# Optimization experiments

Hardware: AMD Instinct MI355X
Metric: run time of the kernel (lower is better)

Reference implementation:

```python
import jax, jax.numpy as jnp
import numpy as np

DIM = 128
HEADS = 4
GN_GROUPS = 4
EPS = 1e-5


def setup_inputs() -> dict:
    key = jax.random.key(0)
    ks = jax.random.split(key, 6)
    B, C, H, W = 4, DIM, 64, 64
    x = jax.random.normal(ks[0], (B, C, H, W), dtype=jnp.float32)
    # 1x1 convs are channel matmuls: store as [out_ch, in_ch]
    w_qkv = jax.random.normal(ks[1], (3 * C, C), dtype=jnp.float32) * (C ** -0.5)
    w_out = jax.random.normal(ks[2], (C, C), dtype=jnp.float32) * (C ** -0.5)
    b_out = jax.random.normal(ks[3], (C,), dtype=jnp.float32) * 0.01
    gn_gamma = jnp.ones((C,), dtype=jnp.float32)
    gn_beta = jnp.zeros((C,), dtype=jnp.float32)
    return {"x": x, "w_qkv": w_qkv, "w_out": w_out, "b_out": b_out,
            "gn_gamma": gn_gamma, "gn_beta": gn_beta}


def _attention_block(x, w_qkv, w_out, b_out, gn_gamma, gn_beta):
    b, c, h, w = x.shape
    d = c // HEADS
    scale = d ** -0.5
    # 1x1 conv == per-pixel matmul over channels
    qkv = jnp.einsum('bchw,oc->bohw', x, w_qkv)  # [b, 3c, h, w]
    q, k, v = jnp.split(qkv, 3, axis=1)
    # 'b (h d) x y -> b h (x y) d'
    def to_heads(t):
        return t.reshape(b, HEADS, d, h * w).transpose(0, 1, 3, 2)  # [b, H, N, d]
    q, k, v = to_heads(q), to_heads(k), to_heads(v)
    dots = jnp.einsum('bhnd,bhmd->bhnm', q, k) * scale  # [b, H, N, N]
    attn = jax.nn.softmax(dots, axis=-1)
    out = jnp.einsum('bhnm,bhmd->bhnd', attn, v)  # [b, H, N, d]
    # 'b h (x y) d -> b (h d) x y'
    out = out.transpose(0, 1, 3, 2).reshape(b, c, h, w)
    # output 1x1 conv + bias
    out = jnp.einsum('bchw,oc->bohw', out, w_out) + b_out[None, :, None, None]
    # GroupNorm(4, c)
    g = out.reshape(b, GN_GROUPS, c // GN_GROUPS, h, w)
    mean = g.mean(axis=(2, 3, 4), keepdims=True)
    var = g.var(axis=(2, 3, 4), keepdims=True)
    g = (g - mean) * jax.lax.rsqrt(var + EPS)
    out = g.reshape(b, c, h, w) * gn_gamma[None, :, None, None] + gn_beta[None, :, None, None]
    return out + x


def reference(x, w_qkv, w_out, b_out, gn_gamma, gn_beta):
    return _attention_block(x, w_qkv, w_out, b_out, gn_gamma, gn_beta)
```

## Files before the change

### kernel.cpp

```cpp
#include <hip/hip_runtime.h>

#define DIM   128
#define NPIX  4096
#define DHEAD 32

using u16 = unsigned short;
typedef __attribute__((ext_vector_type(8))) short   short8;
typedef __attribute__((ext_vector_type(8))) u16     ushort8;
typedef __attribute__((ext_vector_type(4))) float   floatx4;
typedef __attribute__((ext_vector_type(2))) unsigned int uint2v;

#define SCL 0.25513899f

__device__ __forceinline__ float bf2f(u16 u) {
  union { unsigned int i; float f; } v; v.i = ((unsigned int)u) << 16; return v.f;
}
__device__ __forceinline__ u16 f2bf(float f) {
  union { unsigned int i; float f; } v; v.f = f;
  unsigned int i = v.i;
  return (u16)((i + 0x7FFFu + ((i >> 16) & 1u)) >> 16);
}
__device__ __forceinline__ unsigned int pk2bf(float a, float b) {
  union { float f; unsigned int u; } ua, ub; ua.f = a; ub.f = b;
  return __builtin_amdgcn_perm(ub.u, ua.u, 0x07060302u);
}

template<bool F32> __device__ __forceinline__ float ld1(const void* p, size_t i) {
  if constexpr (F32) return ((const float*)p)[i];
  else               return bf2f(((const u16*)p)[i]);
}
template<bool F32> __device__ __forceinline__ float4 ld4(const void* p, size_t i) {
  if constexpr (F32) {
    return *(const float4*)((const float*)p + i);
  } else {
    const ushort4 u = *(const ushort4*)((const u16*)p + i);
    return make_float4(bf2f(u.x), bf2f(u.y), bf2f(u.z), bf2f(u.w));
  }
}
template<bool F32> __device__ __forceinline__ void st4(void* p, size_t i, float4 v) {
  if constexpr (F32) {
    *(float4*)((float*)p + i) = v;
  } else {
    ushort4 u; u.x = f2bf(v.x); u.y = f2bf(v.y); u.z = f2bf(v.z); u.w = f2bf(v.w);
    *(ushort4*)((u16*)p + i) = u;
  }
}

__global__ void k_detect(const u16* __restrict__ x, int* __restrict__ flag,
                         float* __restrict__ S) {
  if (threadIdx.x < 40) S[threadIdx.x] = 0.f;
  if (threadIdx.x == 0 && blockIdx.x == 0) {
    int big = 0;
    for (int i = 0; i < 128; ++i) {
      const float v = bf2f(x[i]);
      if (!(fabsf(v) < 1e4f)) big = 1;
    }
    *flag = big;
  }
}

template<bool F32>
__global__ __launch_bounds__(256) void k_qkv(const void* __restrict__ x,
                                             const void* __restrict__ wqkv,
                                             u16* __restrict__ Q,
                                             u16* __restrict__ K,
                                             u16* __restrict__ V,
                                             const int* __restrict__ flag) {
  if (*flag != (F32 ? 1 : 0)) return;
  const int b = blockIdx.z, y = blockIdx.y, pt = blockIdx.x;
  const int tl = threadIdx.x;
  __shared__ float Ws[32 * 129];
  if (y < 8) {
    const int m = y >> 2, h = y & 3;
    const int ddq = tl & 3, pw = tl >> 2;
    const int rb = m * DIM + h * 32;
    for (int i = tl; i < 32 * DIM; i += 256)
      Ws[(i >> 7) * 129 + (i & 127)] =
          ld1<F32>(wqkv, (size_t)(rb + (i >> 7)) * DIM + (i & 127));
    __syncthreads();
    const int p0 = pt * 256 + pw * 4;
    float acc[8][4];
#pragma unroll
    for (int j = 0; j < 8; ++j) { acc[j][0] = acc[j][1] = acc[j][2] = acc[j][3] = 0.f; }
    const size_t xb = (size_t)b * DIM * NPIX + p0;
    for (int c = 0; c < DIM; ++c) {
      const float4 xv = ld4<F32>(x, xb + (size_t)c * NPIX);
#pragma unroll
      for (int j = 0; j < 8; ++j) {
        const float wv = Ws[(ddq * 8 + j) * 129 + c];
        acc[j][0] += wv * xv.x; acc[j][1] += wv * xv.y;
        acc[j][2] += wv * xv.z; acc[j][3] += wv * xv.w;
      }
    }
    u16* dst = (m == 0) ? Q : K;
    const float scl = (m == 0) ? 1.f : SCL;
    const int bh = b * 4 + h;
#pragma unroll
    for (int t = 0; t < 4; ++t) {
      ushort8 w8;
#pragma unroll
      for (int j = 0; j < 8; ++j) w8[j] = f2bf(acc[j][t] * scl);
      *(ushort8*)(dst + ((size_t)bh * NPIX + p0 + t) * DHEAD + ddq * 8) = w8;
    }
  } else {
    const int og = (y - 8) * 4 + (pt >> 2);
    const int ptv = pt & 3;
    for (int i = tl; i < 8 * DIM; i += 256)
      Ws[(i >> 7) * 129 + (i & 127)] =
          ld1<F32>(wqkv, (size_t)(2 * DIM + og * 8 + (i >> 7)) * DIM + (i & 127));
    __syncthreads();
    const int p0 = ptv * 1024 + tl * 4;
    float acc[8][4];
#pragma unroll
    for (int j = 0; j < 8; ++j) { acc[j][0] = acc[j][1] = acc[j][2] = acc[j][3] = 0.f; }
    const size_t xb = (size_t)b * DIM * NPIX + p0;
    for (int c = 0; c < DIM; ++c) {
      const float4 xv = ld4<F32>(x, xb + (size_t)c * NPIX);
#pragma unroll
      for (int j = 0; j < 8; ++j) {
        const float wv = Ws[j * 129 + c];
        acc[j][0] += wv * xv.x; acc[j][1] += wv * xv.y;
        acc[j][2] += wv * xv.z; acc[j][3] += wv * xv.w;
      }
    }
#pragma unroll
    for (int j = 0; j < 8; ++j) {
      const int c = og * 8 + j;
      ushort4 w4;
      w4.x = f2bf(acc[j][0]); w4.y = f2bf(acc[j][1]);
      w4.z = f2bf(acc[j][2]); w4.w = f2bf(acc[j][3]);
      *(ushort4*)(V + ((size_t)b * DIM + c) * NPIX + p0) = w4;
    }
  }
}

__device__ __forceinline__ short8 xform_p(unsigned c0, unsigned c1,
                                          unsigned c2, unsigned c3) {
  uint2v sw = __builtin_amdgcn_permlane32_swap(c0, c2, false, false);
  uint2v sx = __builtin_amdgcn_permlane16_swap(sw[0], sw[1], false, false);
  uint2v sy = __builtin_amdgcn_permlane32_swap(c1, c3, false, false);
  uint2v sz = __builtin_amdgcn_permlane16_swap(sy[0], sy[1], false, false);
  union { unsigned u[4]; short8 s; } r;
  r.u[0] = sx[0]; r.u[1] = sz[0]; r.u[2] = sx[1]; r.u[3] = sz[1];
  return r.s;
}

__global__ __launch_bounds__(512) void k_attn(const u16* __restrict__ Q,
                                              const u16* __restrict__ K,
                                              const u16* __restrict__ V,
                                              u16* __restrict__ O) {
  const int id = blockIdx.y * 32 + blockIdx.x;
  const int nid = (id & 7) * 64 + (id >> 3);
  const int bh = nid >> 5, qb = nid & 31;
  const int tid = threadIdx.x;
  const int wv = tid >> 6, lane = tid & 63;
  const int quad = lane >> 4, l15 = lane & 15;
  const int b = bh >> 2, h = bh & 3;

  __shared__ __align__(16) u16 Vlds[2][32 * 136];
  __shared__ __align__(16) u16 Olds[32 * 136];

  const int qtok0 = qb * 128 + wv * 16 + l15;
  const short8 qf = *(const short8*)(Q + ((size_t)bh * NPIX + qtok0) * DHEAD + quad * 8);

  floatx4 o00 = {0.f, 0.f, 0.f, 0.f}, o01 = {0.f, 0.f, 0.f, 0.f};
  floatx4 ol  = {0.f, 0.f, 0.f, 0.f};
  const short8 onesf = {(short)0x3F80, (short)0x3F80, (short)0x3F80, (short)0x3F80,
                        (short)0x3F80, (short)0x3F80, (short)0x3F80, (short)0x3F80};

  const u16* Ka = K + ((size_t)bh * NPIX + l15) * DHEAD + quad * 8;

  const int sdd = tid >> 4, soc = tid & 15;
  const u16* Vg = V + ((size_t)(b * DIM + h * DHEAD + sdd)) * NPIX + soc * 8;
  u16* Vd0 = Vlds[0] + sdd * 136 + soc * 8;
  u16* Vd1 = Vlds[1] + sdd * 136 + soc * 8;

  *(ushort8*)Vd0 = *(const ushort8*)Vg;

  for (int ch = 0; ch < 32; ++ch) {
    const int cur = ch & 1;
    ushort8 kf[8];
#pragma unroll
    for (int sub = 0; sub < 8; ++sub)
      kf[sub] = *(const ushort8*)(Ka + (size_t)(ch * 128 + sub * 16) * DHEAD);
    __syncthreads();
    ushort8 vpre;
    if (ch + 1 < 32) vpre = *(const ushort8*)(Vg + (ch + 1) * 128);
#pragma unroll
    for (int kc = 0; kc < 4; ++kc) {
      unsigned ca[4];
#pragma unroll
      for (int s = 0; s < 2; ++s) {
        const int sub = kc * 2 + s;
        union { ushort8 u; short8 s8; } afc; afc.u = kf[sub];
        const floatx4 s0 = __builtin_amdgcn_mfma_f32_16x16x32_bf16(
            afc.s8, qf, (floatx4){0.f, 0.f, 0.f, 0.f}, 0, 0, 0);
        const float a0 = __builtin_amdgcn_exp2f(s0[0]);
        const float a1 = __builtin_amdgcn_exp2f(s0[1]);
        const float a2 = __builtin_amdgcn_exp2f(s0[2]);
        const float a3 = __builtin_amdgcn_exp2f(s0[3]);
        ca[s * 2 + 0] = pk2bf(a0, a1); ca[s * 2 + 1] = pk2bf(a2, a3);
      }
      const short8 pa = xform_p(ca[0], ca[1], ca[2], ca[3]);
      const short8 vb0 = *(const short8*)(Vlds[cur] + l15 * 136 + kc * 32 + quad * 8);
      const short8 vb1 = *(const short8*)(Vlds[cur] + (16 + l15) * 136 + kc * 32 + quad * 8);
      __builtin_amdgcn_s_setprio(1);
      o00 = __builtin_amdgcn_mfma_f32_16x16x32_bf16(pa, vb0, o00, 0, 0, 0);
      o01 = __builtin_amdgcn_mfma_f32_16x16x32_bf16(pa, vb1, o01, 0, 0, 0);
      ol  = __builtin_amdgcn_mfma_f32_16x16x32_bf16(pa, onesf, ol, 0, 0, 0);
      __builtin_amdgcn_s_setprio(0);
    }
    if (ch + 1 < 32) {
      *(ushort8*)(cur ? Vd0 : Vd1) = vpre;
    }
  }
  float li[4];
#pragma unroll
  for (int r = 0; r < 4; ++r) li[r] = 1.f / ol[r];
  uint2v w00, w01;
  w00[0] = (unsigned)f2bf(o00[0] * li[0]) | ((unsigned)f2bf(o00[1] * li[1]) << 16);
  w00[1] = (unsigned)f2bf(o00[2] * li[2]) | ((unsigned)f2bf(o00[3] * li[3]) << 16);
  w01[0] = (unsigned)f2bf(o01[0] * li[0]) | ((unsigned)f2bf(o01[1] * li[1]) << 16);
  w01[1] = (unsigned)f2bf(o01[2] * li[2]) | ((unsigned)f2bf(o01[3] * li[3]) << 16);
  __syncthreads();
  *(uint2v*)(Olds + l15 * 136 + wv * 16 + quad * 4) = w00;
  *(uint2v*)(Olds + (16 + l15) * 136 + wv * 16 + quad * 4) = w01;
  __syncthreads();
  const int d = tid >> 4, oc = tid & 15;
  u16* og = O + ((size_t)(b * DIM + h * DHEAD + d)) * NPIX + qb * 128;
  *(ushort8*)(og + oc * 8) = *(const ushort8*)(Olds + d * 136 + oc * 8);
}

template<bool F32>
__global__ __launch_bounds__(256) void k_proj(const u16* __restrict__ O,
                                              const void* __restrict__ wout,
                                              const void* __restrict__ bout,
                                              float* __restrict__ Y,
                                              float* __restrict__ Sred,
                                              const int* __restrict__ flag) {
  if (*flag != (F32 ? 1 : 0)) return;
  const int b = blockIdx.z, og = blockIdx.y, pt = blockIdx.x;
  const int tl = threadIdx.x;
  __shared__ float Ws[8][DIM];
  __shared__ __align__(16) u16 Olds[2][16][520];
  for (int i = tl; i < 8 * DIM; i += 256)
    Ws[i >> 7][i & 127] = ld1<F32>(wout, (size_t)(og * 8 + (i >> 7)) * DIM + (i & 127));
  const u16* Ob = O + (size_t)b * DIM * NPIX + pt * 512;
  const int srow = tl >> 6;
  const int scol = (tl & 63) * 8;
#pragma unroll
  for (int s = 0; s < 4; ++s) {
    const int r = s * 4 + srow;
    *(ushort8*)(&Olds[0][r][scol]) = *(const ushort8*)(Ob + (size_t)r * NPIX + scol);
  }
  float acc[8][2];
#pragma unroll
  for (int j = 0; j < 8; ++j) { acc[j][0] = acc[j][1] = 0.f; }
  for (int chv = 0; chv < 8; ++chv) {
    const int cur = chv & 1;
    __syncthreads();
    ushort8 pre[4];
    if (chv + 1 < 8) {
      const u16* gb = Ob + (size_t)(chv + 1) * 16 * NPIX;
#pragma unroll
      for (int s = 0; s < 4; ++s)
        pre[s] = *(const ushort8*)(gb + (size_t)(s * 4 + srow) * NPIX + scol);
    }
#pragma unroll
    for (int cc = 0; cc < 16; ++cc) {
      const int c = chv * 16 + cc;
      const ushort2 xv2 = *(const ushort2*)(&Olds[cur][cc][tl * 2]);
      const float x0 = bf2f(xv2.x), x1 = bf2f(xv2.y);
#pragma unroll
      for (int j = 0; j < 8; ++j) {
        const float wv = Ws[j][c];
        acc[j][0] += wv * x0; acc[j][1] += wv * x1;
      }
    }
    if (chv + 1 < 8) {
      const int nxt = cur ^ 1;
#pragma unroll
      for (int s = 0; s < 4; ++s)
        *(ushort8*)(&Olds[nxt][s * 4 + srow][scol]) = pre[s];
    }
  }
  const int p0 = pt * 512 + tl * 2;
  float s1 = 0.f, s2 = 0.f;
#pragma unroll
  for (int j = 0; j < 8; ++j) {
    const int o = og * 8 + j;
    const float bo = ld1<F32>(bout, o);
    float2 y2;
    y2.x = acc[j][0] + bo; y2.y = acc[j][1] + bo;
    *(float2*)(Y + ((size_t)b * DIM + o) * NPIX + p0) = y2;
    s1 += y2.x + y2.y;
    s2 += y2.x * y2.x + y2.y * y2.y;
  }
  __shared__ float red[2][256];
  red[0][tl] = s1; red[1][tl] = s2;
  __syncthreads();
  for (int off = 128; off >= 1; off >>= 1) {
    if (tl < off) { red[0][tl] += red[0][tl + off]; red[1][tl] += red[1][tl + off]; }
    __syncthreads();
  }
  if (tl == 0) {
    const int g = og >> 2;
    atomicAdd(&Sred[(b * 4 + g) * 2 + 0], red[0][0]);
    atomicAdd(&Sred[(b * 4 + g) * 2 + 1], red[1][0]);
  }
}

template<bool F32>
__global__ __launch_bounds__(256) void k_gn(const float* __restrict__ Y,
                                            const float* __restrict__ Sred,
                                            const void* __restrict__ x,
                                            const void* __restrict__ gamma,
                                            const void* __restrict__ beta,
                                            void* __restrict__ out,
                                            const int* __restrict__ flag) {
  if (*flag != (F32 ? 1 : 0)) return;
  const int idx = (blockIdx.x * 256 + threadIdx.x) * 4;
  const int b = idx >> 19;
  const int c = (idx >> 12) & 127;
  const int g = c >> 5;
  const float inv_n = 1.f / (32.f * 4096.f);
  const float s1 = Sred[(b * 4 + g) * 2 + 0];
  const float s2 = Sred[(b * 4 + g) * 2 + 1];
  const float mean = s1 * inv_n;
  const float var = s2 * inv_n - mean * mean;
  const float rs = rsqrtf(var + 1e-5f);
  const float ga = ld1<F32>(gamma, c) * rs;
  const float be = ld1<F32>(beta, c) - mean * ga;
  const float4 y4 = *(const float4*)(Y + idx);
  const float4 xv = ld4<F32>(x, idx);
  float4 r;
  r.x = y4.x * ga + be + xv.x;
  r.y = y4.y * ga + be + xv.y;
  r.z = y4.z * ga + be + xv.z;
  r.w = y4.w * ga + be + xv.w;
  st4<F32>(out, idx, r);
}

extern "C" void kernel_launch(void* const* d_in, const int* in_sizes, int n_in,
                              void* d_out, int out_size, void* d_ws, size_t ws_size,
                              hipStream_t stream) {
  const void* x     = d_in[0];
  const void* wqkv  = d_in[1];
  const void* wout  = d_in[2];
  const void* bout  = d_in[3];
  const void* gamma = d_in[4];
  const void* beta  = d_in[5];
  char* ws = (char*)d_ws;
  u16*   Q = (u16*)(ws + ((size_t)0  << 20));
  u16*   K = (u16*)(ws + ((size_t)8  << 20));
  u16*   V = (u16*)(ws + ((size_t)16 << 20));
  u16*   O = (u16*)(ws + ((size_t)24 << 20));
  float* Y = (float*)(ws + ((size_t)32 << 20));
  float* S = (float*)(ws + ((size_t)40 << 20));
  int*   F = (int*)(ws + ((size_t)40 << 20) + 128);

  k_detect<<<1, 64, 0, stream>>>((const u16*)x, F, S);

  k_qkv<false><<<dim3(16, 12, 4), 256, 0, stream>>>(x, wqkv, Q, K, V, F);
  k_qkv<true> <<<dim3(16, 12, 4), 256, 0, stream>>>(x, wqkv, Q, K, V, F);
  k_attn<<<dim3(32, 16), 512, 0, stream>>>(Q, K, V, O);
  k_proj<false><<<dim3(8, 16, 4), 256, 0, stream>>>(O, wout, bout, Y, S, F);
  k_proj<true> <<<dim3(8, 16, 4), 256, 0, stream>>>(O, wout, bout, Y, S, F);
  k_gn<false><<<2048, 256, 0, stream>>>(Y, S, x, gamma, beta, d_out, F);
  k_gn<true> <<<2048, 256, 0, stream>>>(Y, S, x, gamma, beta, d_out, F);
}
```

Measured before the change: 192.6 us.

## Split attention keys across waves and reduce partial outputs through LDS

The attention kernel previously gave each wave 16 query rows and streamed all keys, with V staged through double-buffered LDS and a barrier every chunk. Now each wave holds all 128 queries of the block in registers and handles its own slice of the keys, reading K and V straight from global memory without LDS staging or per-chunk barriers. The partial outputs and row sums of the eight waves are then added up serially in LDS, with a barrier per wave, before normalisation and the bf16 store. This removes the inner-loop barriers, but it greatly raises register pressure (24 accumulators plus 8 Q fragments), lowers occupancy, and adds a serialized eight-step reduction at the end.

```diff
diff --git a/kernel.cpp b/kernel.cpp
--- a/kernel.cpp
+++ b/kernel.cpp
@@ -157,78 +157,94 @@
   const int quad = lane >> 4, l15 = lane & 15;
   const int b = bh >> 2, h = bh & 3;
 
-  __shared__ __align__(16) u16 Vlds[2][32 * 136];
-  __shared__ __align__(16) u16 Olds[32 * 136];
-
-  const int qtok0 = qb * 128 + wv * 16 + l15;
-  const short8 qf = *(const short8*)(Q + ((size_t)bh * NPIX + qtok0) * DHEAD + quad * 8);
-
-  floatx4 o00 = {0.f, 0.f, 0.f, 0.f}, o01 = {0.f, 0.f, 0.f, 0.f};
-  floatx4 ol  = {0.f, 0.f, 0.f, 0.f};
+  __shared__ __align__(16) float Ob[32][132];
+  __shared__ __align__(16) float Lb[128];
+
+  short8 qf[8];
+#pragma unroll
+  for (int f = 0; f < 8; ++f)
+    qf[f] = *(const short8*)(Q + ((size_t)bh * NPIX + qb * 128 + f * 16 + l15) * DHEAD + quad * 8);
+
+  floatx4 o[8][2], ol[8];
+#pragma unroll
+  for (int f = 0; f < 8; ++f) {
+    o[f][0] = (floatx4){0.f, 0.f, 0.f, 0.f};
+    o[f][1] = (floatx4){0.f, 0.f, 0.f, 0.f};
+    ol[f]   = (floatx4){0.f, 0.f, 0.f, 0.f};
+  }
   const short8 onesf = {(short)0x3F80, (short)0x3F80, (short)0x3F80, (short)0x3F80,
                         (short)0x3F80, (short)0x3F80, (short)0x3F80, (short)0x3F80};
 
-  const u16* Ka = K + ((size_t)bh * NPIX + l15) * DHEAD + quad * 8;
-
-  const int sdd = tid >> 4, soc = tid & 15;
-  const u16* Vg = V + ((size_t)(b * DIM + h * DHEAD + sdd)) * NPIX + soc * 8;
-  u16* Vd0 = Vlds[0] + sdd * 136 + soc * 8;
-  u16* Vd1 = Vlds[1] + sdd * 136 + soc * 8;
-
-  *(ushort8*)Vd0 = *(const ushort8*)Vg;
-
-  for (int ch = 0; ch < 32; ++ch) {
-    const int cur = ch & 1;
-    ushort8 kf[8];
-#pragma unroll
-    for (int sub = 0; sub < 8; ++sub)
-      kf[sub] = *(const ushort8*)(Ka + (size_t)(ch * 128 + sub * 16) * DHEAD);
-    __syncthreads();
-    ushort8 vpre;
-    if (ch + 1 < 32) vpre = *(const ushort8*)(Vg + (ch + 1) * 128);
-#pragma unroll
-    for (int kc = 0; kc < 4; ++kc) {
-      unsigned ca[4];
-#pragma unroll
-      for (int s = 0; s < 2; ++s) {
-        const int sub = kc * 2 + s;
-        union { ushort8 u; short8 s8; } afc; afc.u = kf[sub];
-        const floatx4 s0 = __builtin_amdgcn_mfma_f32_16x16x32_bf16(
-            afc.s8, qf, (floatx4){0.f, 0.f, 0.f, 0.f}, 0, 0, 0);
-        const float a0 = __builtin_amdgcn_exp2f(s0[0]);
-        const float a1 = __builtin_amdgcn_exp2f(s0[1]);
-        const float a2 = __builtin_amdgcn_exp2f(s0[2]);
-        const float a3 = __builtin_amdgcn_exp2f(s0[3]);
-        ca[s * 2 + 0] = pk2bf(a0, a1); ca[s * 2 + 1] = pk2bf(a2, a3);
+  const u16* Kb = K + ((size_t)bh * NPIX + l15) * DHEAD + quad * 8;
+  const u16* Vb = V + ((size_t)(b * DIM + h * DHEAD + l15)) * NPIX + quad * 8;
+
+#pragma unroll 2
+  for (int it = 0; it < 16; ++it) {
+    const int k0 = it * 256 + wv * 32;
+    const short8 af0 = *(const short8*)(Kb + (size_t)k0 * DHEAD);
+    const short8 af1 = *(const short8*)(Kb + (size_t)(k0 + 16) * DHEAD);
+    const short8 vb0 = *(const short8*)(Vb + k0);
+    const short8 vb1 = *(const short8*)(Vb + 16 * NPIX + k0);
+#pragma unroll
+    for (int f = 0; f < 8; ++f) {
+      const floatx4 s0 = __builtin_amdgcn_mfma_f32_16x16x32_bf16(
+          af0, qf[f], (floatx4){0.f, 0.f, 0.f, 0.f}, 0, 0, 0);
+      const floatx4 s1 = __builtin_amdgcn_mfma_f32_16x16x32_bf16(
+          af1, qf[f], (floatx4){0.f, 0.f, 0.f, 0.f}, 0, 0, 0);
+      const float a0 = __builtin_amdgcn_exp2f(s0[0]);
+      const float a1 = __builtin_amdgcn_exp2f(s0[1]);
+      const float a2 = __builtin_amdgcn_exp2f(s0[2]);
+      const float a3 = __builtin_amdgcn_exp2f(s0[3]);
+      const float b0 = __builtin_amdgcn_exp2f(s1[0]);
+      const float b1 = __builtin_amdgcn_exp2f(s1[1]);
+      const float b2 = __builtin_amdgcn_exp2f(s1[2]);
+      const float b3 = __builtin_amdgcn_exp2f(s1[3]);
+      const short8 pa = xform_p(pk2bf(a0, a1), pk2bf(a2, a3),
+                                pk2bf(b0, b1), pk2bf(b2, b3));
+      o[f][0] = __builtin_amdgcn_mfma_f32_16x16x32_bf16(pa, vb0, o[f][0], 0, 0, 0);
+      o[f][1] = __builtin_amdgcn_mfma_f32_16x16x32_bf16(pa, vb1, o[f][1], 0, 0, 0);
+      ol[f]   = __builtin_amdgcn_mfma_f32_16x16x32_bf16(pa, onesf, ol[f], 0, 0, 0);
+    }
+  }
+
+  for (int w = 0; w < 8; ++w) {
+    if (wv == w) {
+      if (w == 0) {
+#pragma unroll
+        for (int f = 0; f < 8; ++f) {
+#pragma unroll
+          for (int t = 0; t < 2; ++t)
+            *(floatx4*)&Ob[t * 16 + l15][f * 16 + quad * 4] = o[f][t];
+          if (l15 == 0) *(floatx4*)&Lb[f * 16 + quad * 4] = ol[f];
+        }
+      } else {
+#pragma unroll
+        for (int f = 0; f < 8; ++f) {
+#pragma unroll
+          for (int t = 0; t < 2; ++t) {
+            floatx4 cu = *(const floatx4*)&Ob[t * 16 + l15][f * 16 + quad * 4];
+            cu = cu + o[f][t];
+            *(floatx4*)&Ob[t * 16 + l15][f * 16 + quad * 4] = cu;
+          }
+          if (l15 == 0) {
+            floatx4 cl = *(const floatx4*)&Lb[f * 16 + quad * 4];
+            cl = cl + ol[f];
+            *(floatx4*)&Lb[f * 16 + quad * 4] = cl;
+          }
+        }
       }
-      const short8 pa = xform_p(ca[0], ca[1], ca[2], ca[3]);
-      const short8 vb0 = *(const short8*)(Vlds[cur] + l15 * 136 + kc * 32 + quad * 8);
-      const short8 vb1 = *(const short8*)(Vlds[cur] + (16 + l15) * 136 + kc * 32 + quad * 8);
-      __builtin_amdgcn_s_setprio(1);
-      o00 = __builtin_amdgcn_mfma_f32_16x16x32_bf16(pa, vb0, o00, 0, 0, 0);
-      o01 = __builtin_amdgcn_mfma_f32_16x16x32_bf16(pa, vb1, o01, 0, 0, 0);
-      ol  = __builtin_amdgcn_mfma_f32_16x16x32_bf16(pa, onesf, ol, 0, 0, 0);
-      __builtin_amdgcn_s_setprio(0);
-    }
-    if (ch + 1 < 32) {
-      *(ushort8*)(cur ? Vd0 : Vd1) = vpre;
-    }
-  }
-  float li[4];
-#pragma unroll
-  for (int r = 0; r < 4; ++r) li[r] = 1.f / ol[r];
-  uint2v w00, w01;
-  w00[0] = (unsigned)f2bf(o00[0] * li[0]) | ((unsigned)f2bf(o00[1] * li[1]) << 16);
-  w00[1] = (unsigned)f2bf(o00[2] * li[2]) | ((unsigned)f2bf(o00[3] * li[3]) << 16);
-  w01[0] = (unsigned)f2bf(o01[0] * li[0]) | ((unsigned)f2bf(o01[1] * li[1]) << 16);
-  w01[1] = (unsigned)f2bf(o01[2] * li[2]) | ((unsigned)f2bf(o01[3] * li[3]) << 16);
-  __syncthreads();
-  *(uint2v*)(Olds + l15 * 136 + wv * 16 + quad * 4) = w00;
-  *(uint2v*)(Olds + (16 + l15) * 136 + wv * 16 + quad * 4) = w01;
-  __syncthreads();
-  const int d = tid >> 4, oc = tid & 15;
-  u16* og = O + ((size_t)(b * DIM + h * DHEAD + d)) * NPIX + qb * 128;
-  *(ushort8*)(og + oc * 8) = *(const ushort8*)(Olds + d * 136 + oc * 8);
+    }
+    __syncthreads();
+  }
+
+  const int dd = tid >> 4, q8 = (tid & 15) * 8;
+  ushort8 w8;
+#pragma unroll
+  for (int j = 0; j < 8; ++j) {
+    const float li = 1.f / Lb[q8 + j];
+    w8[j] = f2bf(Ob[dd][q8 + j] * li);
+  }
+  *(ushort8*)(O + ((size_t)(b * DIM + h * DHEAD + dd)) * NPIX + qb * 128 + q8) = w8;
 }
 
 template<bool F32>
```

After: 199.0 us. 3.3% more time.

## Switch attention to 32x32x16 MFMA tiles with K staged in LDS

Applied to the files above, without the earlier changes.

Rewrites the attention kernel so each wave handles 32 query rows with 32x32x16 bf16 MFMAs instead of 16x16x32. Blocks drop from 512 to 256 threads, and K is now double-buffered in LDS alongside V rather than loaded straight from global into registers. The P-fragment shuffle needs only permlane32 swaps, and the output is written in wider 16-element chunks. Larger tiles give more reuse of each loaded fragment and fewer permute instructions, at the cost of more accumulator registers, extra LDS, and fewer waves per block.

```diff
diff --git a/kernel.cpp b/kernel.cpp
--- a/kernel.cpp
+++ b/kernel.cpp
@@ -8,6 +8,7 @@
 typedef __attribute__((ext_vector_type(8))) short   short8;
 typedef __attribute__((ext_vector_type(8))) u16     ushort8;
 typedef __attribute__((ext_vector_type(4))) float   floatx4;
+typedef __attribute__((ext_vector_type(16))) float  floatx16;
 typedef __attribute__((ext_vector_type(2))) unsigned int uint2v;
 
 #define SCL 0.25513899f
@@ -134,18 +135,7 @@
   }
 }
 
-__device__ __forceinline__ short8 xform_p(unsigned c0, unsigned c1,
-                                          unsigned c2, unsigned c3) {
-  uint2v sw = __builtin_amdgcn_permlane32_swap(c0, c2, false, false);
-  uint2v sx = __builtin_amdgcn_permlane16_swap(sw[0], sw[1], false, false);
-  uint2v sy = __builtin_amdgcn_permlane32_swap(c1, c3, false, false);
-  uint2v sz = __builtin_amdgcn_permlane16_swap(sy[0], sy[1], false, false);
-  union { unsigned u[4]; short8 s; } r;
-  r.u[0] = sx[0]; r.u[1] = sz[0]; r.u[2] = sx[1]; r.u[3] = sz[1];
-  return r.s;
-}
-
-__global__ __launch_bounds__(512) void k_attn(const u16* __restrict__ Q,
+__global__ __launch_bounds__(256) void k_attn(const u16* __restrict__ Q,
                                               const u16* __restrict__ K,
                                               const u16* __restrict__ V,
                                               u16* __restrict__ O) {
@@ -154,81 +144,101 @@
   const int bh = nid >> 5, qb = nid & 31;
   const int tid = threadIdx.x;
   const int wv = tid >> 6, lane = tid & 63;
-  const int quad = lane >> 4, l15 = lane & 15;
+  const int l31 = lane & 31, hl = lane >> 5;
   const int b = bh >> 2, h = bh & 3;
 
+  __shared__ __align__(16) u16 Klds[2][128 * 40];
   __shared__ __align__(16) u16 Vlds[2][32 * 136];
   __shared__ __align__(16) u16 Olds[32 * 136];
 
-  const int qtok0 = qb * 128 + wv * 16 + l15;
-  const short8 qf = *(const short8*)(Q + ((size_t)bh * NPIX + qtok0) * DHEAD + quad * 8);
-
-  floatx4 o00 = {0.f, 0.f, 0.f, 0.f}, o01 = {0.f, 0.f, 0.f, 0.f};
-  floatx4 ol  = {0.f, 0.f, 0.f, 0.f};
+  const int qtok = qb * 128 + wv * 32 + l31;
+  const u16* qp = Q + ((size_t)bh * NPIX + qtok) * DHEAD + hl * 8;
+  const short8 qf0 = *(const short8*)(qp);
+  const short8 qf1 = *(const short8*)(qp + 16);
+
+  floatx16 ocr = {0.f,0.f,0.f,0.f,0.f,0.f,0.f,0.f,0.f,0.f,0.f,0.f,0.f,0.f,0.f,0.f};
+  floatx16 olr = {0.f,0.f,0.f,0.f,0.f,0.f,0.f,0.f,0.f,0.f,0.f,0.f,0.f,0.f,0.f,0.f};
+  const floatx16 z16 = {0.f,0.f,0.f,0.f,0.f,0.f,0.f,0.f,0.f,0.f,0.f,0.f,0.f,0.f,0.f,0.f};
   const short8 onesf = {(short)0x3F80, (short)0x3F80, (short)0x3F80, (short)0x3F80,
                         (short)0x3F80, (short)0x3F80, (short)0x3F80, (short)0x3F80};
 
-  const u16* Ka = K + ((size_t)bh * NPIX + l15) * DHEAD + quad * 8;
-
-  const int sdd = tid >> 4, soc = tid & 15;
-  const u16* Vg = V + ((size_t)(b * DIM + h * DHEAD + sdd)) * NPIX + soc * 8;
-  u16* Vd0 = Vlds[0] + sdd * 136 + soc * 8;
-  u16* Vd1 = Vlds[1] + sdd * 136 + soc * 8;
-
-  *(ushort8*)Vd0 = *(const ushort8*)Vg;
+  const int skey = tid >> 1, shf = tid & 1;
+  const int sdd = tid >> 3, soc = tid & 7;
+  const u16* Kg = K + ((size_t)bh * NPIX + skey) * DHEAD + shf * 16;
+  const u16* Vg = V + ((size_t)(b * DIM + h * DHEAD + sdd)) * NPIX + soc * 16;
+  u16* Kd0 = Klds[0] + skey * 40 + shf * 16;
+  u16* Kd1 = Klds[1] + skey * 40 + shf * 16;
+  u16* Vd0 = Vlds[0] + sdd * 136 + soc * 16;
+  u16* Vd1 = Vlds[1] + sdd * 136 + soc * 16;
+
+  *(ushort8*)(Kd0)     = *(const ushort8*)(Kg);
+  *(ushort8*)(Kd0 + 8) = *(const ushort8*)(Kg + 8);
+  *(ushort8*)(Vd0)     = *(const ushort8*)(Vg);
+  *(ushort8*)(Vd0 + 8) = *(const ushort8*)(Vg + 8);
 
   for (int ch = 0; ch < 32; ++ch) {
     const int cur = ch & 1;
-    ushort8 kf[8];
-#pragma unroll
-    for (int sub = 0; sub < 8; ++sub)
-      kf[sub] = *(const ushort8*)(Ka + (size_t)(ch * 128 + sub * 16) * DHEAD);
-    __syncthreads();
-    ushort8 vpre;
-    if (ch + 1 < 32) vpre = *(const ushort8*)(Vg + (ch + 1) * 128);
-#pragma unroll
-    for (int kc = 0; kc < 4; ++kc) {
-      unsigned ca[4];
-#pragma unroll
-      for (int s = 0; s < 2; ++s) {
-        const int sub = kc * 2 + s;
-        union { ushort8 u; short8 s8; } afc; afc.u = kf[sub];
-        const floatx4 s0 = __builtin_amdgcn_mfma_f32_16x16x32_bf16(
-            afc.s8, qf, (floatx4){0.f, 0.f, 0.f, 0.f}, 0, 0, 0);
-        const float a0 = __builtin_amdgcn_exp2f(s0[0]);
-        const float a1 = __builtin_amdgcn_exp2f(s0[1]);
-        const float a2 = __builtin_amdgcn_exp2f(s0[2]);
-        const float a3 = __builtin_amdgcn_exp2f(s0[3]);
-        ca[s * 2 + 0] = pk2bf(a0, a1); ca[s * 2 + 1] = pk2bf(a2, a3);
-      }
-      const short8 pa = xform_p(ca[0], ca[1], ca[2], ca[3]);
-      const short8 vb0 = *(const short8*)(Vlds[cur] + l15 * 136 + kc * 32 + quad * 8);
-      const short8 vb1 = *(const short8*)(Vlds[cur] + (16 + l15) * 136 + kc * 32 + quad * 8);
+    __syncthreads();
+    ushort8 kp0, kp1, vp0, vp1;
+    if (ch + 1 < 32) {
+      const u16* kg = Kg + (size_t)(ch + 1) * 128 * DHEAD;
+      const u16* vg = Vg + (ch + 1) * 128;
+      kp0 = *(const ushort8*)kg; kp1 = *(const ushort8*)(kg + 8);
+      vp0 = *(const ushort8*)vg; vp1 = *(const ushort8*)(vg + 8);
+    }
+#pragma unroll
+    for (int kb = 0; kb < 4; ++kb) {
+      const u16* kr = Klds[cur] + (kb * 32 + l31) * 40 + hl * 8;
+      const short8 af0 = *(const short8*)(kr);
+      const short8 af1 = *(const short8*)(kr + 16);
+      floatx16 sc = __builtin_amdgcn_mfma_f32_32x32x16_bf16(af0, qf0, z16, 0, 0, 0);
+      sc = __builtin_amdgcn_mfma_f32_32x32x16_bf16(af1, qf1, sc, 0, 0, 0);
+      float p[16];
+#pragma unroll
+      for (int r = 0; r < 16; ++r) p[r] = __builtin_amdgcn_exp2f(sc[r]);
+      const unsigned d0 = pk2bf(p[0],  p[1]),  d1 = pk2bf(p[2],  p[3]);
+      const unsigned d2 = pk2bf(p[4],  p[5]),  d3 = pk2bf(p[6],  p[7]);
+      const unsigned d4 = pk2bf(p[8],  p[9]),  d5 = pk2bf(p[10], p[11]);
+      const unsigned d6 = pk2bf(p[12], p[13]), d7 = pk2bf(p[14], p[15]);
+      const uint2v sA = __builtin_amdgcn_permlane32_swap(d0, d2, false, false);
+      const uint2v sB = __builtin_amdgcn_permlane32_swap(d1, d3, false, false);
+      const uint2v sC = __builtin_amdgcn_permlane32_swap(d4, d6, false, false);
+      const uint2v sD = __builtin_amdgcn_permlane32_swap(d5, d7, false, false);
+      union { unsigned u[4]; short8 s; } f0, f1;
+      f0.u[0] = sA[0]; f0.u[1] = sB[0]; f0.u[2] = sA[1]; f0.u[3] = sB[1];
+      f1.u[0] = sC[0]; f1.u[1] = sD[0]; f1.u[2] = sC[1]; f1.u[3] = sD[1];
+      const u16* vr = Vlds[cur] + l31 * 136 + kb * 32 + hl * 8;
+      const short8 vb0 = *(const short8*)(vr);
+      const short8 vb1 = *(const short8*)(vr + 16);
       __builtin_amdgcn_s_setprio(1);
-      o00 = __builtin_amdgcn_mfma_f32_16x16x32_bf16(pa, vb0, o00, 0, 0, 0);
-      o01 = __builtin_amdgcn_mfma_f32_16x16x32_bf16(pa, vb1, o01, 0, 0, 0);
-      ol  = __builtin_amdgcn_mfma_f32_16x16x32_bf16(pa, onesf, ol, 0, 0, 0);
+      ocr = __builtin_amdgcn_mfma_f32_32x32x16_bf16(f0.s, vb0, ocr, 0, 0, 0);
+      ocr = __builtin_amdgcn_mfma_f32_32x32x16_bf16(f1.s, vb1, ocr, 0, 0, 0);
+      olr = __builtin_amdgcn_mfma_f32_32x32x16_bf16(f0.s, onesf, olr, 0, 0, 0);
+      olr = __builtin_amdgcn_mfma_f32_32x32x16_bf16(f1.s, onesf, olr, 0, 0, 0);
       __builtin_amdgcn_s_setprio(0);
     }
     if (ch + 1 < 32) {
-      *(ushort8*)(cur ? Vd0 : Vd1) = vpre;
-    }
-  }
-  float li[4];
-#pragma unroll
-  for (int r = 0; r < 4; ++r) li[r] = 1.f / ol[r];
-  uint2v w00, w01;
-  w00[0] = (unsigned)f2bf(o00[0] * li[0]) | ((unsigned)f2bf(o00[1] * li[1]) << 16);
-  w00[1] = (unsigned)f2bf(o00[2] * li[2]) | ((unsigned)f2bf(o00[3] * li[3]) << 16);
-  w01[0] = (unsigned)f2bf(o01[0] * li[0]) | ((unsigned)f2bf(o01[1] * li[1]) << 16);
-  w01[1] = (unsigned)f2bf(o01[2] * li[2]) | ((unsigned)f2bf(o01[3] * li[3]) << 16);
+      u16* kd = cur ? Kd0 : Kd1;
+      u16* vd = cur ? Vd0 : Vd1;
+      *(ushort8*)(kd)     = kp0; *(ushort8*)(kd + 8) = kp1;
+      *(ushort8*)(vd)     = vp0; *(ushort8*)(vd + 8) = vp1;
+    }
+  }
+#pragma unroll
+  for (int rr = 0; rr < 4; ++rr) {
+    const float i0 = 1.f / olr[rr * 4 + 0], i1 = 1.f / olr[rr * 4 + 1];
+    const float i2 = 1.f / olr[rr * 4 + 2], i3 = 1.f / olr[rr * 4 + 3];
+    uint2v w;
+    w[0] = (unsigned)f2bf(ocr[rr * 4 + 0] * i0) | ((unsigned)f2bf(ocr[rr * 4 + 1] * i1) << 16);
+    w[1] = (unsigned)f2bf(ocr[rr * 4 + 2] * i2) | ((unsigned)f2bf(ocr[rr * 4 + 3] * i3) << 16);
+    *(uint2v*)(Olds + l31 * 136 + wv * 32 + rr * 8 + hl * 4) = w;
+  }
   __syncthreads();
-  *(uint2v*)(Olds + l15 * 136 + wv * 16 + quad * 4) = w00;
-  *(uint2v*)(Olds + (16 + l15) * 136 + wv * 16 + quad * 4) = w01;
-  __syncthreads();
-  const int d = tid >> 4, oc = tid & 15;
-  u16* og = O + ((size_t)(b * DIM + h * DHEAD + d)) * NPIX + qb * 128;
-  *(ushort8*)(og + oc * 8) = *(const ushort8*)(Olds + d * 136 + oc * 8);
+  const int dd = tid >> 3, oc8 = tid & 7;
+  u16* og = O + ((size_t)(b * DIM + h * DHEAD + dd)) * NPIX + qb * 128 + oc8 * 16;
+  const u16* orow = Olds + dd * 136 + oc8 * 16;
+  *(ushort8*)(og)     = *(const ushort8*)(orow);
+  *(ushort8*)(og + 8) = *(const ushort8*)(orow + 8);
 }
 
 template<bool F32>
@@ -363,7 +373,7 @@
 
   k_qkv<false><<<dim3(16, 12, 4), 256, 0, stream>>>(x, wqkv, Q, K, V, F);
   k_qkv<true> <<<dim3(16, 12, 4), 256, 0, stream>>>(x, wqkv, Q, K, V, F);
-  k_attn<<<dim3(32, 16), 512, 0, stream>>>(Q, K, V, O);
+  k_attn<<<dim3(32, 16), 256, 0, stream>>>(Q, K, V, O);
   k_proj<false><<<dim3(8, 16, 4), 256, 0, stream>>>(O, wout, bout, Y, S, F);
   k_proj<true> <<<dim3(8, 16, 4), 256, 0, stream>>>(O, wout, bout, Y, S, F);
   k_gn<false><<<2048, 256, 0, stream>>>(Y, S, x, gamma, beta, d_out, F);
```

Measured after the change: 188.5 us. -2.1%, faster.
